# Optimization experiments

Hardware: AMD Instinct MI355X
Metric: run time of the kernel (lower is better)

## Reference

```python
import jax, jax.numpy as jnp
import numpy as np

B, K, C = 8, 16384, 256
NPROP, NSAMPLE, RADIUS = 1024, 16, 0.3
NUM_CLASS, NH, NS = 18, 12, 18
DOUT = 2 + 3 + NH * 2 + NS * 4 + NUM_CLASS  # 119


def setup_inputs() -> dict:
    key = jax.random.key(0)
    ks = jax.random.split(key, 16)
    w = lambda k, shape: jax.random.normal(k, shape, jnp.float32) * 0.05
    return {
        "xyz": jax.random.uniform(ks[0], (B, K, 3), jnp.float32) * 4.0,
        "features": jax.random.normal(ks[1], (B, C, K), jnp.float32),
        # SA shared-MLP (conv2d 1x1) weights, BN folded to scale/bias (inference)
        "W1": w(ks[2], (128, C + 3)), "g1": jnp.ones((128,), jnp.float32), "b1": jnp.zeros((128,), jnp.float32),
        "W2": w(ks[3], (128, 128)),   "g2": jnp.ones((128,), jnp.float32), "b2": jnp.zeros((128,), jnp.float32),
        "W3": w(ks[4], (128, 128)),   "g3": jnp.ones((128,), jnp.float32), "b3": jnp.zeros((128,), jnp.float32),
        # proposal head conv1d stack
        "P1": w(ks[5], (128, 128)),  "pg1": jnp.ones((128,), jnp.float32), "pb1": jnp.zeros((128,), jnp.float32),
        "P2": w(ks[6], (128, 128)),  "pg2": jnp.ones((128,), jnp.float32), "pb2": jnp.zeros((128,), jnp.float32),
        "P3": w(ks[7], (DOUT, 128)), "pb3": jnp.zeros((DOUT,), jnp.float32),
        "mean_size_arr": jnp.abs(jax.random.normal(ks[8], (NS, 3), jnp.float32)) + 0.5,
    }


def fps(xyz, npoint):
    """Farthest point sampling. xyz: [B,K,3] -> [B,npoint] int32."""
    Bn, Kn, _ = xyz.shape
    def step(carry, _):
        dist, far = carry                                   # [B,K], [B]
        sel = jnp.take_along_axis(xyz, far[:, None, None], axis=1)  # [B,1,3]
        d = jnp.sum((xyz - sel) ** 2, axis=-1)              # [B,K]
        dist = jnp.minimum(dist, d)
        return (dist, jnp.argmax(dist, axis=-1).astype(jnp.int32)), far
    init = (jnp.full((Bn, Kn), 1e10, xyz.dtype), jnp.zeros((Bn,), jnp.int32))
    _, inds = jax.lax.scan(step, init, None, length=npoint)  # [npoint,B]
    return inds.T


def ball_query(new_xyz, xyz, radius, nsample):
    """First nsample points within radius of each center (pad with first hit)."""
    Kn = xyz.shape[1]
    d2 = jnp.sum((new_xyz[:, :, None, :] - xyz[:, None, :, :]) ** 2, axis=-1)  # [B,P,K]
    idx = jnp.where(d2 < radius * radius, jnp.arange(Kn, dtype=jnp.int32)[None, None, :], Kn)
    idx = jnp.sort(idx, axis=-1)[..., :nsample]             # first hits in index order
    first = idx[..., :1]                                    # center itself is always a hit
    return jnp.where(idx == Kn, first, idx).astype(jnp.int32)


def reference(xyz, features, W1, g1, b1, W2, g2, b2, W3, g3, b3,
              P1, pg1, pb1, P2, pg2, pb2, P3, pb3, mean_size_arr):
    Bn = xyz.shape[0]
    fps_idx = fps(xyz, NPROP)                                           # [B,P]
    new_xyz = jnp.take_along_axis(xyz, fps_idx[:, :, None], axis=1)     # [B,P,3]
    idx = ball_query(new_xyz, xyz, RADIUS, NSAMPLE)                     # [B,P,S]
    flat = idx.reshape(Bn, -1)
    g_xyz = jnp.take_along_axis(xyz, flat[:, :, None], axis=1).reshape(Bn, NPROP, NSAMPLE, 3)
    g_xyz = (g_xyz - new_xyz[:, :, None, :]) / RADIUS                   # normalize_xyz=True
    f = jnp.swapaxes(features, 1, 2)                                    # [B,K,C]
    g_feat = jnp.take_along_axis(f, flat[:, :, None], axis=1).reshape(Bn, NPROP, NSAMPLE, C)
    x = jnp.concatenate([g_xyz, g_feat], axis=-1)                       # [B,P,S,C+3] (use_xyz)
    for Wl, gl, bl in ((W1, g1, b1), (W2, g2, b2), (W3, g3, b3)):
        x = jax.nn.relu(jnp.einsum('bpsc,oc->bpso', x, Wl) * gl + bl)
    feat = jnp.max(x, axis=2)                                           # [B,P,128] max-pool over ball
    h = jax.nn.relu(jnp.einsum('bpc,oc->bpo', feat, P1) * pg1 + pb1)
    h = jax.nn.relu(jnp.einsum('bpc,oc->bpo', h, P2) * pg2 + pb2)
    net = jnp.einsum('bpc,oc->bpo', h, P3) + pb3                        # [B,P,119]
    # decode_scores slicing
    obj = net[:, :, 0:2]
    center = new_xyz + net[:, :, 2:5]
    heading_scores = net[:, :, 5:5 + NH]
    heading_residuals = net[:, :, 5 + NH:5 + 2 * NH] * (np.pi / NH)
    size_scores = net[:, :, 5 + 2 * NH:5 + 2 * NH + NS]
    srn = net[:, :, 5 + 2 * NH + NS:5 + 2 * NH + 4 * NS].reshape(Bn, NPROP, NS, 3)
    size_residuals = srn * mean_size_arr[None, None]
    sem_cls_scores = net[:, :, 5 + 2 * NH + 4 * NS:]
    return (obj, center, heading_scores, heading_residuals, size_scores,
            size_residuals, sem_cls_scores, feat)
```

## Files before the change

### kernel.cpp

```cpp
#include <hip/hip_runtime.h>
#include <math.h>

static constexpr int BB = 8;
static constexpr int KK = 16384;
static constexpr int CC = 256;
static constexpr int NPROP = 1024;
static constexpr int NSAMP = 16;
static constexpr int NH = 12;
static constexpr int NS = 18;
static constexpr int NCLS = 18;
static constexpr int DOUT = 119;

static constexpr int OFF_OBJ = 0;
static constexpr int OFF_CEN = OFF_OBJ + BB * NPROP * 2;
static constexpr int OFF_HS  = OFF_CEN + BB * NPROP * 3;
static constexpr int OFF_HR  = OFF_HS + BB * NPROP * NH;
static constexpr int OFF_SS  = OFF_HR + BB * NPROP * NH;
static constexpr int OFF_SR  = OFF_SS + BB * NPROP * NS;
static constexpr int OFF_SC  = OFF_SR + BB * NPROP * NS * 3;
static constexpr int OFF_FEAT = OFF_SC + BB * NPROP * NCLS;

__global__ void prep_weights(const float* __restrict__ W1, const float* __restrict__ W2,
                             const float* __restrict__ W3, const float* __restrict__ P1,
                             const float* __restrict__ P2, const float* __restrict__ P3,
                             float* __restrict__ W1T, float* __restrict__ W2T,
                             float* __restrict__ W3T, float* __restrict__ P1T,
                             float* __restrict__ P2T, float* __restrict__ P3T) {
    int i = blockIdx.x * 256 + threadIdx.x;
    if (i < 260 * 128) {
        int c = i >> 7, o = i & 127;
        W1T[i] = (c < 259) ? W1[o * 259 + c] : 0.f;
        return;
    }
    i -= 260 * 128;
    if (i < 16384) { int c = i >> 7, o = i & 127; W2T[i] = W2[o * 128 + c]; return; }
    i -= 16384;
    if (i < 16384) { int c = i >> 7, o = i & 127; W3T[i] = W3[o * 128 + c]; return; }
    i -= 16384;
    if (i < 16384) { int c = i >> 7, o = i & 127; P1T[i] = P1[o * 128 + c]; return; }
    i -= 16384;
    if (i < 16384) { int c = i >> 7, o = i & 127; P2T[i] = P2[o * 128 + c]; return; }
    i -= 16384;
    if (i < 128 * DOUT) { int c = i / DOUT, o = i % DOUT; P3T[i] = P3[o * 128 + c]; return; }
}

__global__ __launch_bounds__(256) void transpose_feat(const float* __restrict__ f,
                                                      float* __restrict__ fT) {
    __shared__ float tile[32][33];
    int b = blockIdx.z;
    int k0 = blockIdx.x * 32, c0 = blockIdx.y * 32;
    int tx = threadIdx.x, ty = threadIdx.y;
    const float* fb = f + (size_t)b * CC * KK;
#pragma unroll
    for (int i = 0; i < 4; i++) {
        int cl = ty + i * 8;
        tile[cl][tx] = fb[(size_t)(c0 + cl) * KK + k0 + tx];
    }
    __syncthreads();
    float* fTb = fT + (size_t)b * KK * CC;
#pragma unroll
    for (int i = 0; i < 4; i++) {
        int kl = ty + i * 8;
        fTb[(size_t)(k0 + kl) * CC + c0 + tx] = tile[tx][kl];
    }
}

__global__ __launch_bounds__(1024) void fps_kernel(const float* __restrict__ xyz,
                                                   int* __restrict__ fps_idx,
                                                   float* __restrict__ new_xyz) {
#pragma clang fp contract(off)
    int b = blockIdx.x;
    int tid = threadIdx.x;
    int lane = tid & 63, wid = tid >> 6;
    const float* xb = xyz + (size_t)b * KK * 3;

    float px[16], py[16], pz[16], dist[16];
#pragma unroll
    for (int j = 0; j < 16; j++) {
        int idx = j * 1024 + tid;
        px[j] = xb[idx * 3 + 0];
        py[j] = xb[idx * 3 + 1];
        pz[j] = xb[idx * 3 + 2];
        dist[j] = 1e10f;
    }
    __shared__ float redv[16];
    __shared__ int redi[16];
    __shared__ int curslot;
    int cur = 0;
    for (int t = 0; t < NPROP; t++) {
        float sx = xb[cur * 3 + 0];
        float sy = xb[cur * 3 + 1];
        float sz = xb[cur * 3 + 2];
        if (tid == 0) {
            fps_idx[b * NPROP + t] = cur;
            new_xyz[(b * NPROP + t) * 3 + 0] = sx;
            new_xyz[(b * NPROP + t) * 3 + 1] = sy;
            new_xyz[(b * NPROP + t) * 3 + 2] = sz;
        }
        float lmax = -1.f;
        int lidx = 0;
#pragma unroll
        for (int j = 0; j < 16; j++) {
            float dx = px[j] - sx;
            float dy = py[j] - sy;
            float dz = pz[j] - sz;
            float a = dx * dx;
            float bq = dy * dy;
            float cq = dz * dz;
            float d = (a + bq) + cq;
            float nd = dist[j] < d ? dist[j] : d;
            dist[j] = nd;
            if (nd > lmax) { lmax = nd; lidx = j * 1024 + tid; }
        }
#pragma unroll
        for (int m = 1; m < 64; m <<= 1) {
            float ov = __shfl_xor(lmax, m, 64);
            int oi = __shfl_xor(lidx, m, 64);
            if (ov > lmax || (ov == lmax && oi < lidx)) { lmax = ov; lidx = oi; }
        }
        if (lane == 0) { redv[wid] = lmax; redi[wid] = lidx; }
        __syncthreads();
        if (wid == 0) {
            float v = lane < 16 ? redv[lane] : -2.f;
            int i2 = lane < 16 ? redi[lane] : 0x7fffffff;
#pragma unroll
            for (int m = 1; m < 16; m <<= 1) {
                float ov = __shfl_xor(v, m, 64);
                int oi = __shfl_xor(i2, m, 64);
                if (ov > v || (ov == v && oi < i2)) { v = ov; i2 = oi; }
            }
            if (lane == 0) curslot = i2;
        }
        __syncthreads();
        cur = curslot;
    }
}

__global__ __launch_bounds__(256) void ballquery_kernel(const float* __restrict__ xyz,
                                                        const float* __restrict__ new_xyz,
                                                        int* __restrict__ bq) {
#pragma clang fp contract(off)
    int gid = blockIdx.x * 4 + (threadIdx.x >> 6);
    int lane = threadIdx.x & 63;
    int b = gid >> 10, p = gid & 1023;
    const float* xb = xyz + (size_t)b * KK * 3;
    float cx = new_xyz[(b * NPROP + p) * 3 + 0];
    float cy = new_xyz[(b * NPROP + p) * 3 + 1];
    float cz = new_xyz[(b * NPROP + p) * 3 + 2];
    const float R2 = (float)(0.3 * 0.3);
    int out_base = (b * NPROP + p) * NSAMP;
    int found = 0;
    int firsthit = -1;
    for (int base = 0; base < KK && found < NSAMP; base += 64) {
        int k = base + lane;
        float dx = cx - xb[k * 3 + 0];
        float dy = cy - xb[k * 3 + 1];
        float dz = cz - xb[k * 3 + 2];
        float a = dx * dx;
        float bb2 = dy * dy;
        float cc2 = dz * dz;
        float d2 = (a + bb2) + cc2;
        bool pred = d2 < R2;
        unsigned long long mask = __ballot(pred);
        int prefix = __popcll(mask & ((1ull << lane) - 1ull));
        if (pred) {
            int pos = found + prefix;
            if (pos < NSAMP) bq[out_base + pos] = k;
        }
        if (firsthit < 0 && mask) firsthit = base + (__ffsll(mask) - 1);
        found += __popcll(mask);
    }
    if (lane < NSAMP && lane >= found) bq[out_base + lane] = firsthit;
}

__global__ __launch_bounds__(256) void fused_mlp(
    const float* __restrict__ fT, const float* __restrict__ xyz,
    const float* __restrict__ new_xyz, const int* __restrict__ bq,
    const float* __restrict__ W1T, const float* __restrict__ g1, const float* __restrict__ b1,
    const float* __restrict__ W2T, const float* __restrict__ g2, const float* __restrict__ b2,
    const float* __restrict__ W3T, const float* __restrict__ g3, const float* __restrict__ b3,
    const float* __restrict__ P1T, const float* __restrict__ pg1, const float* __restrict__ pb1,
    const float* __restrict__ P2T, const float* __restrict__ pg2, const float* __restrict__ pb2,
    const float* __restrict__ P3T, const float* __restrict__ pb3, const float* __restrict__ msa,
    float* __restrict__ out) {
    __shared__ float xs[16][260];
    __shared__ float hA[16][128];
    __shared__ float hB[16][128];
    __shared__ float pmax[8][128];
    __shared__ float featl[128];
    __shared__ float heada[128];
    __shared__ float headb[128];
    __shared__ int sidx[16];

    int tid = threadIdx.x;
    int blk = blockIdx.x;
    int b = blk >> 10, p = blk & 1023;
    int bp = b * NPROP + p;

    if (tid < 16) sidx[tid] = bq[bp * NSAMP + tid];
    float c0 = new_xyz[bp * 3 + 0];
    float c1 = new_xyz[bp * 3 + 1];
    float c2 = new_xyz[bp * 3 + 2];
    __syncthreads();

    for (int s = 0; s < 16; s++) {
        int k = sidx[s];
        xs[s][3 + tid] = fT[((size_t)(b * KK + k)) * CC + tid];
        if (tid < 3) {
            float xv = xyz[((size_t)(b * KK + k)) * 3 + tid];
            float cv = (tid == 0) ? c0 : (tid == 1) ? c1 : c2;
            xs[s][tid] = (xv - cv) / 0.3f;
        }
        if (tid == 3) xs[s][259] = 0.f;
    }
    __syncthreads();

    int og = tid & 31, sg = tid >> 5;
    int o0 = og * 4, s0 = sg * 2;
    float acc[4][2];

#pragma unroll
    for (int oi = 0; oi < 4; oi++) { acc[oi][0] = 0.f; acc[oi][1] = 0.f; }
    for (int cg = 0; cg < 65; cg++) {
        int cb = cg * 4;
        float wv[4][4], xv[2][4];
#pragma unroll
        for (int j = 0; j < 4; j++)
            *(float4*)&wv[j][0] = *(const float4*)&W1T[(cb + j) * 128 + o0];
        *(float4*)&xv[0][0] = *(const float4*)&xs[s0][cb];
        *(float4*)&xv[1][0] = *(const float4*)&xs[s0 + 1][cb];
#pragma unroll
        for (int j = 0; j < 4; j++)
#pragma unroll
            for (int oi = 0; oi < 4; oi++) {
                acc[oi][0] += wv[j][oi] * xv[0][j];
                acc[oi][1] += wv[j][oi] * xv[1][j];
            }
    }
    {
        float ga[4], ba[4];
        *(float4*)ga = *(const float4*)&g1[o0];
        *(float4*)ba = *(const float4*)&b1[o0];
#pragma unroll
        for (int si = 0; si < 2; si++) {
            float tmp[4];
#pragma unroll
            for (int oi = 0; oi < 4; oi++)
                tmp[oi] = fmaxf(acc[oi][si] * ga[oi] + ba[oi], 0.f);
            *(float4*)&hA[s0 + si][o0] = *(float4*)tmp;
        }
    }
    __syncthreads();

#pragma unroll
    for (int oi = 0; oi < 4; oi++) { acc[oi][0] = 0.f; acc[oi][1] = 0.f; }
    for (int cg = 0; cg < 32; cg++) {
        int cb = cg * 4;
        float wv[4][4], xv[2][4];
#pragma unroll
        for (int j = 0; j < 4; j++)
            *(float4*)&wv[j][0] = *(const float4*)&W2T[(cb + j) * 128 + o0];
        *(float4*)&xv[0][0] = *(const float4*)&hA[s0][cb];
        *(float4*)&xv[1][0] = *(const float4*)&hA[s0 + 1][cb];
#pragma unroll
        for (int j = 0; j < 4; j++)
#pragma unroll
            for (int oi = 0; oi < 4; oi++) {
                acc[oi][0] += wv[j][oi] * xv[0][j];
                acc[oi][1] += wv[j][oi] * xv[1][j];
            }
    }
    {
        float ga[4], ba[4];
        *(float4*)ga = *(const float4*)&g2[o0];
        *(float4*)ba = *(const float4*)&b2[o0];
#pragma unroll
        for (int si = 0; si < 2; si++) {
            float tmp[4];
#pragma unroll
            for (int oi = 0; oi < 4; oi++)
                tmp[oi] = fmaxf(acc[oi][si] * ga[oi] + ba[oi], 0.f);
            *(float4*)&hB[s0 + si][o0] = *(float4*)tmp;
        }
    }
    __syncthreads();

#pragma unroll
    for (int oi = 0; oi < 4; oi++) { acc[oi][0] = 0.f; acc[oi][1] = 0.f; }
    for (int cg = 0; cg < 32; cg++) {
        int cb = cg * 4;
        float wv[4][4], xv[2][4];
#pragma unroll
        for (int j = 0; j < 4; j++)
            *(float4*)&wv[j][0] = *(const float4*)&W3T[(cb + j) * 128 + o0];
        *(float4*)&xv[0][0] = *(const float4*)&hB[s0][cb];
        *(float4*)&xv[1][0] = *(const float4*)&hB[s0 + 1][cb];
#pragma unroll
        for (int j = 0; j < 4; j++)
#pragma unroll
            for (int oi = 0; oi < 4; oi++) {
                acc[oi][0] += wv[j][oi] * xv[0][j];
                acc[oi][1] += wv[j][oi] * xv[1][j];
            }
    }
    {
        float ga[4], ba[4];
        *(float4*)ga = *(const float4*)&g3[o0];
        *(float4*)ba = *(const float4*)&b3[o0];
        float tmp[4];
#pragma unroll
        for (int oi = 0; oi < 4; oi++) {
            float v0 = fmaxf(acc[oi][0] * ga[oi] + ba[oi], 0.f);
            float v1 = fmaxf(acc[oi][1] * ga[oi] + ba[oi], 0.f);
            tmp[oi] = fmaxf(v0, v1);
        }
        *(float4*)&pmax[sg][o0] = *(float4*)tmp;
    }
    __syncthreads();

    if (tid < 128) {
        float m = pmax[0][tid];
#pragma unroll
        for (int s = 1; s < 8; s++) m = fmaxf(m, pmax[s][tid]);
        featl[tid] = m;
        out[OFF_FEAT + (size_t)bp * 128 + tid] = m;
    }
    __syncthreads();

    if (tid < 128) {
        float s = 0.f;
        for (int c = 0; c < 128; c++) s += P1T[c * 128 + tid] * featl[c];
        heada[tid] = fmaxf(s * pg1[tid] + pb1[tid], 0.f);
    }
    __syncthreads();
    if (tid < 128) {
        float s = 0.f;
        for (int c = 0; c < 128; c++) s += P2T[c * 128 + tid] * heada[c];
        headb[tid] = fmaxf(s * pg2[tid] + pb2[tid], 0.f);
    }
    __syncthreads();
    if (tid < DOUT) {
        float s = 0.f;
        for (int c = 0; c < 128; c++) s += P3T[c * DOUT + tid] * headb[c];
        s += pb3[tid];
        if (tid < 2) {
            out[OFF_OBJ + (size_t)bp * 2 + tid] = s;
        } else if (tid < 5) {
            out[OFF_CEN + (size_t)bp * 3 + (tid - 2)] = new_xyz[bp * 3 + (tid - 2)] + s;
        } else if (tid < 17) {
            out[OFF_HS + (size_t)bp * NH + (tid - 5)] = s;
        } else if (tid < 29) {
            out[OFF_HR + (size_t)bp * NH + (tid - 17)] = s * (float)(M_PI / 12.0);
        } else if (tid < 47) {
            out[OFF_SS + (size_t)bp * NS + (tid - 29)] = s;
        } else if (tid < 101) {
            int j = tid - 47;
            out[OFF_SR + (size_t)bp * NS * 3 + j] = s * msa[j];
        } else {
            out[OFF_SC + (size_t)bp * NCLS + (tid - 101)] = s;
        }
    }
}

extern "C" void kernel_launch(void* const* d_in, const int* in_sizes, int n_in,
                              void* d_out, int out_size, void* d_ws, size_t ws_size,
                              hipStream_t stream) {
    const float* xyz = (const float*)d_in[0];
    const float* features = (const float*)d_in[1];
    const float* W1 = (const float*)d_in[2];
    const float* g1 = (const float*)d_in[3];
    const float* b1 = (const float*)d_in[4];
    const float* W2 = (const float*)d_in[5];
    const float* g2 = (const float*)d_in[6];
    const float* b2 = (const float*)d_in[7];
    const float* W3 = (const float*)d_in[8];
    const float* g3 = (const float*)d_in[9];
    const float* b3 = (const float*)d_in[10];
    const float* P1 = (const float*)d_in[11];
    const float* pg1 = (const float*)d_in[12];
    const float* pb1 = (const float*)d_in[13];
    const float* P2 = (const float*)d_in[14];
    const float* pg2 = (const float*)d_in[15];
    const float* pb2 = (const float*)d_in[16];
    const float* P3 = (const float*)d_in[17];
    const float* pb3 = (const float*)d_in[18];
    const float* msa = (const float*)d_in[19];
    float* out = (float*)d_out;

    char* w = (char*)d_ws;
    float* W1T = (float*)w; w += (size_t)260 * 128 * 4;
    float* W2T = (float*)w; w += 16384 * 4;
    float* W3T = (float*)w; w += 16384 * 4;
    float* P1T = (float*)w; w += 16384 * 4;
    float* P2T = (float*)w; w += 16384 * 4;
    float* P3T = (float*)w; w += 16384 * 4;
    int* fps_i = (int*)w;  w += (size_t)BB * NPROP * 4;
    float* nxyz = (float*)w; w += (size_t)BB * NPROP * 3 * 4;
    int* bq = (int*)w;     w += (size_t)BB * NPROP * NSAMP * 4;
    float* fT = (float*)w; w += (size_t)BB * KK * CC * 4;

    int prep_elems = 260 * 128 + 16384 * 4 + 128 * DOUT;
    prep_weights<<<(prep_elems + 255) / 256, 256, 0, stream>>>(
        W1, W2, W3, P1, P2, P3, W1T, W2T, W3T, P1T, P2T, P3T);
    transpose_feat<<<dim3(KK / 32, CC / 32, BB), dim3(32, 8), 0, stream>>>(features, fT);
    fps_kernel<<<BB, 1024, 0, stream>>>(xyz, fps_i, nxyz);
    ballquery_kernel<<<(BB * NPROP) / 4, 256, 0, stream>>>(xyz, nxyz, bq);
    fused_mlp<<<BB * NPROP, 256, 0, stream>>>(
        fT, xyz, nxyz, bq,
        W1T, g1, b1, W2T, g2, b2, W3T, g3, b3,
        P1T, pg1, pb1, P2T, pg2, pb2, P3T, pb3, msa, out);
}
```

Baseline: 3.070 ms.

## Fuse FPS, feature transpose and weight prep into one concurrent launch

Merges farthest-point sampling, the feature transpose and the weight transposes into a single kernel whose blocks branch on block index. The transpose and weight-prep work can then run on idle CUs while the 8 serial FPS blocks execute, instead of in separate, serialized launches. The transpose tile grows to 64x64 with 1024 threads, and the unused fps index output is dropped. There is some risk that the shared 1024-thread launch bounds constrain FPS register allocation.

```diff
diff --git a/kernel.cpp b/kernel.cpp
--- a/kernel.cpp
+++ b/kernel.cpp
@@ -10,6 +10,8 @@
 static constexpr int NS = 18;
 static constexpr int NCLS = 18;
 static constexpr int DOUT = 119;
+static constexpr int NTT = 8192;
+static constexpr int NPREP = 112;
 
 static constexpr int OFF_OBJ = 0;
 static constexpr int OFF_CEN = OFF_OBJ + BB * NPROP * 2;
@@ -20,119 +22,127 @@
 static constexpr int OFF_SC  = OFF_SR + BB * NPROP * NS * 3;
 static constexpr int OFF_FEAT = OFF_SC + BB * NPROP * NCLS;
 
-__global__ void prep_weights(const float* __restrict__ W1, const float* __restrict__ W2,
-                             const float* __restrict__ W3, const float* __restrict__ P1,
-                             const float* __restrict__ P2, const float* __restrict__ P3,
-                             float* __restrict__ W1T, float* __restrict__ W2T,
-                             float* __restrict__ W3T, float* __restrict__ P1T,
-                             float* __restrict__ P2T, float* __restrict__ P3T) {
-    int i = blockIdx.x * 256 + threadIdx.x;
-    if (i < 260 * 128) {
-        int c = i >> 7, o = i & 127;
-        W1T[i] = (c < 259) ? W1[o * 259 + c] : 0.f;
+__global__ __launch_bounds__(1024, 4) void stage1(
+    const float* __restrict__ xyz, const float* __restrict__ features,
+    const float* __restrict__ W1, const float* __restrict__ W2, const float* __restrict__ W3,
+    const float* __restrict__ P1, const float* __restrict__ P2, const float* __restrict__ P3,
+    float* __restrict__ fT, float* __restrict__ W1T, float* __restrict__ W2T,
+    float* __restrict__ W3T, float* __restrict__ P1T, float* __restrict__ P2T,
+    float* __restrict__ P3T, float* __restrict__ new_xyz) {
+#pragma clang fp contract(off)
+    __shared__ union {
+        float t[64 * 65];
+        struct { float redv[16]; int redi[16]; int curslot; } r;
+    } sm;
+    int tid = threadIdx.x;
+    int blk = blockIdx.x;
+
+    if (blk < BB) {
+        const int b = blk;
+        const int lane = tid & 63, wid = tid >> 6;
+        const float* xb = xyz + (size_t)b * KK * 3;
+
+        float px[16], py[16], pz[16], dist[16];
+#pragma unroll
+        for (int j = 0; j < 16; j++) {
+            int idx = j * 1024 + tid;
+            px[j] = xb[idx * 3 + 0];
+            py[j] = xb[idx * 3 + 1];
+            pz[j] = xb[idx * 3 + 2];
+            dist[j] = 1e10f;
+        }
+        int cur = 0;
+        for (int t = 0; t < NPROP; t++) {
+            float sx = xb[cur * 3 + 0];
+            float sy = xb[cur * 3 + 1];
+            float sz = xb[cur * 3 + 2];
+            if (tid == 0) {
+                size_t o = ((size_t)b * NPROP + t) * 3;
+                new_xyz[o + 0] = sx;
+                new_xyz[o + 1] = sy;
+                new_xyz[o + 2] = sz;
+            }
+            float lmax = -1.f;
+            int lidx = 0;
+#pragma unroll
+            for (int j = 0; j < 16; j++) {
+                float dx = px[j] - sx;
+                float dy = py[j] - sy;
+                float dz = pz[j] - sz;
+                float a = dx * dx;
+                float bq = dy * dy;
+                float cq = dz * dz;
+                float d = (a + bq) + cq;
+                float nd = dist[j] < d ? dist[j] : d;
+                dist[j] = nd;
+                if (nd > lmax) { lmax = nd; lidx = j * 1024 + tid; }
+            }
+#pragma unroll
+            for (int m = 1; m < 64; m <<= 1) {
+                float ov = __shfl_xor(lmax, m, 64);
+                int oi = __shfl_xor(lidx, m, 64);
+                if (ov > lmax || (ov == lmax && oi < lidx)) { lmax = ov; lidx = oi; }
+            }
+            if (lane == 0) { sm.r.redv[wid] = lmax; sm.r.redi[wid] = lidx; }
+            __syncthreads();
+            if (wid == 0) {
+                float v = lane < 16 ? sm.r.redv[lane] : -2.f;
+                int i2 = lane < 16 ? sm.r.redi[lane] : 0x7fffffff;
+#pragma unroll
+                for (int m = 1; m < 16; m <<= 1) {
+                    float ov = __shfl_xor(v, m, 64);
+                    int oi = __shfl_xor(i2, m, 64);
+                    if (ov > v || (ov == v && oi < i2)) { v = ov; i2 = oi; }
+                }
+                if (lane == 0) sm.r.curslot = i2;
+            }
+            __syncthreads();
+            cur = sm.r.curslot;
+        }
         return;
     }
-    i -= 260 * 128;
-    if (i < 16384) { int c = i >> 7, o = i & 127; W2T[i] = W2[o * 128 + c]; return; }
-    i -= 16384;
-    if (i < 16384) { int c = i >> 7, o = i & 127; W3T[i] = W3[o * 128 + c]; return; }
-    i -= 16384;
-    if (i < 16384) { int c = i >> 7, o = i & 127; P1T[i] = P1[o * 128 + c]; return; }
-    i -= 16384;
-    if (i < 16384) { int c = i >> 7, o = i & 127; P2T[i] = P2[o * 128 + c]; return; }
-    i -= 16384;
-    if (i < 128 * DOUT) { int c = i / DOUT, o = i % DOUT; P3T[i] = P3[o * 128 + c]; return; }
-}
-
-__global__ __launch_bounds__(256) void transpose_feat(const float* __restrict__ f,
-                                                      float* __restrict__ fT) {
-    __shared__ float tile[32][33];
-    int b = blockIdx.z;
-    int k0 = blockIdx.x * 32, c0 = blockIdx.y * 32;
-    int tx = threadIdx.x, ty = threadIdx.y;
-    const float* fb = f + (size_t)b * CC * KK;
-#pragma unroll
-    for (int i = 0; i < 4; i++) {
-        int cl = ty + i * 8;
-        tile[cl][tx] = fb[(size_t)(c0 + cl) * KK + k0 + tx];
-    }
-    __syncthreads();
-    float* fTb = fT + (size_t)b * KK * CC;
-#pragma unroll
-    for (int i = 0; i < 4; i++) {
-        int kl = ty + i * 8;
-        fTb[(size_t)(k0 + kl) * CC + c0 + tx] = tile[tx][kl];
-    }
-}
-
-__global__ __launch_bounds__(1024) void fps_kernel(const float* __restrict__ xyz,
-                                                   int* __restrict__ fps_idx,
-                                                   float* __restrict__ new_xyz) {
-#pragma clang fp contract(off)
-    int b = blockIdx.x;
-    int tid = threadIdx.x;
-    int lane = tid & 63, wid = tid >> 6;
-    const float* xb = xyz + (size_t)b * KK * 3;
-
-    float px[16], py[16], pz[16], dist[16];
-#pragma unroll
-    for (int j = 0; j < 16; j++) {
-        int idx = j * 1024 + tid;
-        px[j] = xb[idx * 3 + 0];
-        py[j] = xb[idx * 3 + 1];
-        pz[j] = xb[idx * 3 + 2];
-        dist[j] = 1e10f;
-    }
-    __shared__ float redv[16];
-    __shared__ int redi[16];
-    __shared__ int curslot;
-    int cur = 0;
-    for (int t = 0; t < NPROP; t++) {
-        float sx = xb[cur * 3 + 0];
-        float sy = xb[cur * 3 + 1];
-        float sz = xb[cur * 3 + 2];
-        if (tid == 0) {
-            fps_idx[b * NPROP + t] = cur;
-            new_xyz[(b * NPROP + t) * 3 + 0] = sx;
-            new_xyz[(b * NPROP + t) * 3 + 1] = sy;
-            new_xyz[(b * NPROP + t) * 3 + 2] = sz;
-        }
-        float lmax = -1.f;
-        int lidx = 0;
-#pragma unroll
-        for (int j = 0; j < 16; j++) {
-            float dx = px[j] - sx;
-            float dy = py[j] - sy;
-            float dz = pz[j] - sz;
-            float a = dx * dx;
-            float bq = dy * dy;
-            float cq = dz * dz;
-            float d = (a + bq) + cq;
-            float nd = dist[j] < d ? dist[j] : d;
-            dist[j] = nd;
-            if (nd > lmax) { lmax = nd; lidx = j * 1024 + tid; }
-        }
-#pragma unroll
-        for (int m = 1; m < 64; m <<= 1) {
-            float ov = __shfl_xor(lmax, m, 64);
-            int oi = __shfl_xor(lidx, m, 64);
-            if (ov > lmax || (ov == lmax && oi < lidx)) { lmax = ov; lidx = oi; }
-        }
-        if (lane == 0) { redv[wid] = lmax; redi[wid] = lidx; }
+    blk -= BB;
+
+    if (blk < NTT) {
+        int bz = blk >> 10;
+        int t2 = blk & 1023;
+        int k0 = (t2 & 255) << 6;
+        int c0 = (t2 >> 8) << 6;
+        int tx = tid & 63, ty = tid >> 6;
+        const float* fb = features + (size_t)bz * CC * KK;
+#pragma unroll
+        for (int i = 0; i < 4; i++) {
+            int c = ty + (i << 4);
+            sm.t[c * 65 + tx] = fb[(size_t)(c0 + c) * KK + k0 + tx];
+        }
         __syncthreads();
-        if (wid == 0) {
-            float v = lane < 16 ? redv[lane] : -2.f;
-            int i2 = lane < 16 ? redi[lane] : 0x7fffffff;
-#pragma unroll
-            for (int m = 1; m < 16; m <<= 1) {
-                float ov = __shfl_xor(v, m, 64);
-                int oi = __shfl_xor(i2, m, 64);
-                if (ov > v || (ov == v && oi < i2)) { v = ov; i2 = oi; }
-            }
-            if (lane == 0) curslot = i2;
-        }
-        __syncthreads();
-        cur = curslot;
+        float* fTb = fT + (size_t)bz * KK * CC;
+#pragma unroll
+        for (int i = 0; i < 4; i++) {
+            int k = ty + (i << 4);
+            fTb[(size_t)(k0 + k) * CC + c0 + tx] = sm.t[tx * 65 + k];
+        }
+        return;
+    }
+    blk -= NTT;
+
+    {
+        int i = blk * 1024 + tid;
+        if (i < 260 * 128) {
+            int c = i >> 7, o = i & 127;
+            W1T[i] = (c < 259) ? W1[o * 259 + c] : 0.f;
+            return;
+        }
+        i -= 260 * 128;
+        if (i < 16384) { int c = i >> 7, o = i & 127; W2T[i] = W2[o * 128 + c]; return; }
+        i -= 16384;
+        if (i < 16384) { int c = i >> 7, o = i & 127; W3T[i] = W3[o * 128 + c]; return; }
+        i -= 16384;
+        if (i < 16384) { int c = i >> 7, o = i & 127; P1T[i] = P1[o * 128 + c]; return; }
+        i -= 16384;
+        if (i < 16384) { int c = i >> 7, o = i & 127; P2T[i] = P2[o * 128 + c]; return; }
+        i -= 16384;
+        if (i < 128 * DOUT) { int c = i / DOUT, o = i % DOUT; P3T[i] = P3[o * 128 + c]; return; }
     }
 }
 
@@ -394,16 +404,13 @@
     float* P1T = (float*)w; w += 16384 * 4;
     float* P2T = (float*)w; w += 16384 * 4;
     float* P3T = (float*)w; w += 16384 * 4;
-    int* fps_i = (int*)w;  w += (size_t)BB * NPROP * 4;
     float* nxyz = (float*)w; w += (size_t)BB * NPROP * 3 * 4;
     int* bq = (int*)w;     w += (size_t)BB * NPROP * NSAMP * 4;
     float* fT = (float*)w; w += (size_t)BB * KK * CC * 4;
 
-    int prep_elems = 260 * 128 + 16384 * 4 + 128 * DOUT;
-    prep_weights<<<(prep_elems + 255) / 256, 256, 0, stream>>>(
-        W1, W2, W3, P1, P2, P3, W1T, W2T, W3T, P1T, P2T, P3T);
-    transpose_feat<<<dim3(KK / 32, CC / 32, BB), dim3(32, 8), 0, stream>>>(features, fT);
-    fps_kernel<<<BB, 1024, 0, stream>>>(xyz, fps_i, nxyz);
+    stage1<<<BB + NTT + NPREP, 1024, 0, stream>>>(
+        xyz, features, W1, W2, W3, P1, P2, P3,
+        fT, W1T, W2T, W3T, P1T, P2T, P3T, nxyz);
     ballquery_kernel<<<(BB * NPROP) / 4, 256, 0, stream>>>(xyz, nxyz, bq);
     fused_mlp<<<BB * NPROP, 256, 0, stream>>>(
         fT, xyz, nxyz, bq,
```

New measurement: 3.301 ms. +7.5%, slower.
